# Optimization experiments

Measured on AMD Instinct MI355X. Metric: run time of the kernel, lower is better.

## Reference

```python
import jax, jax.numpy as jnp
import numpy as np

N_NODES = 50000


def _sage_max(x, src, dst, W_l, b_l, W_r):
    # gather neighbor (source) features, scatter-max to destination nodes
    msgs = x[src]                                   # [E, F]
    agg = jax.ops.segment_max(msgs, dst, num_segments=N_NODES)  # [N, F], -inf for empty
    agg = jnp.where(jnp.isneginf(agg), 0.0, agg)    # PyG fills isolated nodes with 0
    return agg @ W_l + b_l + x @ W_r                # lin_l(aggr) + lin_r(x)


def setup_inputs() -> dict:
    key = jax.random.key(0)
    ks = jax.random.split(key, 9)
    F_IN, H, OUT, E, EL = 128, 256, 32, 800000, 200000
    x = jax.random.normal(ks[0], (N_NODES, F_IN), dtype=jnp.float32)
    edge_index = jax.random.randint(ks[1], (2, E), 0, N_NODES, dtype=jnp.int64)
    edge_label_index = jax.random.randint(ks[2], (2, EL), 0, N_NODES, dtype=jnp.int64)
    s1 = 1.0 / np.sqrt(F_IN)
    s2 = 1.0 / np.sqrt(H)
    W1_l = jax.random.normal(ks[3], (F_IN, H), dtype=jnp.float32) * s1
    b1 = jnp.zeros((H,), dtype=jnp.float32)
    W1_r = jax.random.normal(ks[4], (F_IN, H), dtype=jnp.float32) * s1
    W2_l = jax.random.normal(ks[5], (H, OUT), dtype=jnp.float32) * s2
    b2 = jnp.zeros((OUT,), dtype=jnp.float32)
    W2_r = jax.random.normal(ks[6], (H, OUT), dtype=jnp.float32) * s2
    return {"x": x, "edge_index": edge_index, "edge_label_index": edge_label_index,
            "W1_l": W1_l, "b1": b1, "W1_r": W1_r,
            "W2_l": W2_l, "b2": b2, "W2_r": W2_r}


def reference(x, edge_index, edge_label_index, W1_l, b1, W1_r, W2_l, b2, W2_r):
    src, dst = edge_index[0], edge_index[1]
    # encode (eval mode: dropout is identity)
    h = jax.nn.relu(_sage_max(x, src, dst, W1_l, b1, W1_r))
    z = _sage_max(h, src, dst, W2_l, b2, W2_r)       # [N, 32]
    # decode: dot product between endpoint embeddings
    s = z[edge_label_index[0]]
    d = z[edge_label_index[1]]
    return jnp.sum(s * d, axis=-1)                   # [E_label]
```

## Files before the change

kernel.cpp:

```cpp
#include <hip/hip_runtime.h>
#include <hip/hip_bf16.h>
#include <math.h>

#define N_NODES 50000
#define NBKT 196
#define BSH 8
#define TILE2 4096
#define CAP 64
#define P2CAP 5888
#define SCAN_FLAG 0x40000000

typedef __attribute__((ext_vector_type(8))) short short8;
typedef __attribute__((ext_vector_type(4))) float f32x4;

static __device__ __forceinline__ float b2f(unsigned int u16) {
    union { unsigned int i; float f; } c; c.i = u16 << 16; return c.f;
}
static __device__ __forceinline__ unsigned int fbits(float f) {
    union { float f; unsigned int i; } c; c.f = f; return c.i;
}
static __device__ __forceinline__ unsigned short f2b_rne(float f) {
    unsigned int u = fbits(f);
    u += 0x7fff + ((u >> 16) & 1);
    return (unsigned short)(u >> 16);
}

static __device__ __forceinline__ unsigned char quant8(float v) {
    int q = (int)(v * 15.9375f + 0.5f);
    return (unsigned char)min(q, 255);
}
static __device__ __forceinline__ float dequant8(int b) {
    return (float)b * 0.0627451f;
}


__global__ __launch_bounds__(256) void k_prepbin(
        const float* __restrict__ x, unsigned short* __restrict__ xb,
        const float* __restrict__ W1l, const float* __restrict__ W1r, unsigned short* __restrict__ wt1,
        const float* __restrict__ W2l, const float* __restrict__ W2r, unsigned short* __restrict__ wt2,
        const int* __restrict__ src, const int* __restrict__ dst, int E,
        uint2* __restrict__ tmp, int* __restrict__ cnts, int ntile) {
    __shared__ int cnt[256], sstart[256], lcur[256];
    __shared__ uint2 stage[TILE2];
    const int CX = (N_NODES * 128 / 4) / 256;
    const int CW = CX + 320;
    int b = blockIdx.x, t = threadIdx.x;
    if (b < CX) {
        int i = b * 256 + t;
        float4 v = *(const float4*)(x + (size_t)i * 4);
        ushort4 o;
        o.x = f2b_rne(v.x); o.y = f2b_rne(v.y); o.z = f2b_rne(v.z); o.w = f2b_rne(v.w);
        *(ushort4*)(xb + (size_t)i * 4) = o;
    } else if (b < CX + 256) {
        int i = (b - CX) * 256 + t;
        int n = i >> 8, k = i & 255;
        float v = (k < 128) ? W1l[(size_t)k * 256 + n] : W1r[(size_t)(k - 128) * 256 + n];
        wt1[(size_t)n * 256 + k] = f2b_rne(v);
    } else if (b < CW) {
        int i = (b - CX - 256) * 256 + t;
        int n = i >> 9, k = i & 511;
        float v = (k < 256) ? W2l[(size_t)k * 32 + n] : W2r[(size_t)(k - 256) * 32 + n];
        wt2[(size_t)n * 512 + k] = f2b_rne(v);
    } else {
        int tb = b - CW;
        int e0 = tb * TILE2;
        int tilecnt = min(TILE2, E - e0);
        if (tilecnt <= 0) return;
        cnt[t] = 0;
        __syncthreads();
        if (tilecnt == TILE2) {
            for (int i = 4 * t; i < TILE2; i += 1024) {
                int4 d = *(const int4*)(dst + e0 + i);
                atomicAdd(&cnt[d.x >> BSH], 1);
                atomicAdd(&cnt[d.y >> BSH], 1);
                atomicAdd(&cnt[d.z >> BSH], 1);
                atomicAdd(&cnt[d.w >> BSH], 1);
            }
        } else {
            for (int i = t; i < tilecnt; i += 256)
                atomicAdd(&cnt[dst[e0 + i] >> BSH], 1);
        }
        __syncthreads();
        int cv = cnt[t];
        sstart[t] = cv;
        __syncthreads();
        for (int off = 1; off < 256; off <<= 1) {
            int add = (t >= off) ? sstart[t - off] : 0;
            __syncthreads();
            sstart[t] += add;
            __syncthreads();
        }
        int mystart = sstart[t] - cv;
        __syncthreads();
        sstart[t] = mystart;
        lcur[t] = mystart;
        __syncthreads();
        if (tilecnt == TILE2) {
            for (int i = 4 * t; i < TILE2; i += 1024) {
                int4 d = *(const int4*)(dst + e0 + i);
                int4 s = *(const int4*)(src + e0 + i);
                int q0 = atomicAdd(&lcur[d.x >> BSH], 1); stage[q0] = (uint2){(unsigned)s.x, (unsigned)d.x};
                int q1 = atomicAdd(&lcur[d.y >> BSH], 1); stage[q1] = (uint2){(unsigned)s.y, (unsigned)d.y};
                int q2 = atomicAdd(&lcur[d.z >> BSH], 1); stage[q2] = (uint2){(unsigned)s.z, (unsigned)d.z};
                int q3 = atomicAdd(&lcur[d.w >> BSH], 1); stage[q3] = (uint2){(unsigned)s.w, (unsigned)d.w};
            }
        } else {
            for (int i = t; i < tilecnt; i += 256) {
                int d = dst[e0 + i];
                int s = src[e0 + i];
                int q = atomicAdd(&lcur[d >> BSH], 1);
                uint2 p; p.x = (unsigned)s; p.y = (unsigned)d;
                stage[q] = p;
            }
        }
        __syncthreads();
        if (t < NBKT) cnts[(size_t)t * ntile + tb] = cnt[t];
        for (int i = t; i < tilecnt; i += 256) {
            uint2 p = stage[i];
            int bk = (int)(p.y >> BSH);
            tmp[((size_t)bk * ntile + tb) * CAP + (i - sstart[bk])] = p;
        }
    }
}


__global__ __launch_bounds__(256) void k_bin2(const uint2* __restrict__ tmp,
        const int* __restrict__ cnts, int* __restrict__ pub,
        int* __restrict__ rowptr, int* __restrict__ esrc, int N, int E, int ntile) {
    __shared__ int sc[256], toff[260], nodecnt[256], lcur[256];
    __shared__ int stage[P2CAP];
    __shared__ int shsum[4];
    int k = blockIdx.x, t = threadIdx.x;

    int c = (t < ntile) ? cnts[(size_t)k * ntile + t] : 0;
    sc[t] = c;
    __syncthreads();
    for (int off = 1; off < 256; off <<= 1) {
        int add = (t >= off) ? sc[t - off] : 0;
        __syncthreads();
        sc[t] += add;
        __syncthreads();
    }
    if (t < ntile) toff[t] = sc[t] - c;
    if (t == 255) toff[ntile] = sc[255];
    __syncthreads();
    int total = toff[ntile];

    if (t == 255) atomicExch(&pub[k], SCAN_FLAG | total);
    int v = 0;
    if (t < k) {
        int val;
        do { val = atomicOr(&pub[t], 0); } while (!(val & SCAN_FLAG) || (val & 0x80000000));
        v = val & (SCAN_FLAG - 1);
    }
#pragma unroll
    for (int off = 32; off >= 1; off >>= 1) v += __shfl_xor(v, off);
    if ((t & 63) == 0) shsum[t >> 6] = v;
    nodecnt[t] = 0;
    __syncthreads();
    int base = shsum[0] + shsum[1] + shsum[2] + shsum[3];

    for (int i = t; i < total; i += 256) {
        int lo = 0, hi = ntile;
        while (hi - lo > 1) { int mid = (lo + hi) >> 1; if (toff[mid] <= i) lo = mid; else hi = mid; }
        uint2 p = tmp[((size_t)k * ntile + lo) * CAP + (i - toff[lo])];
        atomicAdd(&nodecnt[(int)p.y & 255], 1);
    }
    __syncthreads();

    int nc = nodecnt[t];
    sc[t] = nc;
    __syncthreads();
    for (int off = 1; off < 256; off <<= 1) {
        int add = (t >= off) ? sc[t - off] : 0;
        __syncthreads();
        sc[t] += add;
        __syncthreads();
    }
    int ex = sc[t] - nc;
    int node = (k << BSH) + t;
    if (node < N) rowptr[node] = base + ex;
    if (node == N) rowptr[N] = E;
    lcur[t] = ex;
    __syncthreads();

    if (total <= P2CAP) {
        for (int i = t; i < total; i += 256) {
            int lo = 0, hi = ntile;
            while (hi - lo > 1) { int mid = (lo + hi) >> 1; if (toff[mid] <= i) lo = mid; else hi = mid; }
            uint2 p = tmp[((size_t)k * ntile + lo) * CAP + (i - toff[lo])];
            int q = atomicAdd(&lcur[(int)p.y & 255], 1);
            stage[q] = (int)p.x;
        }
        __syncthreads();
        for (int i = t; i < total; i += 256)
            esrc[base + i] = stage[i];
    } else {
        for (int i = t; i < total; i += 256) {
            int lo = 0, hi = ntile;
            while (hi - lo > 1) { int mid = (lo + hi) >> 1; if (toff[mid] <= i) lo = mid; else hi = mid; }
            uint2 p = tmp[((size_t)k * ntile + lo) * CAP + (i - toff[lo])];
            int q = atomicAdd(&lcur[(int)p.y & 255], 1);
            esrc[base + q] = (int)p.x;
        }
    }
}


__global__ __launch_bounds__(256) void k_seg_max1(const unsigned short* __restrict__ feat,
        const int* __restrict__ rowptr, const int* __restrict__ esrc,
        unsigned short* __restrict__ out) {
    int w = threadIdx.x >> 6, t = threadIdx.x & 63;
    int n = blockIdx.x * 4 + w;
    int lane16 = t & 15, sub = t >> 4;
    int beg = rowptr[n], end = rowptr[n + 1];
    float m[8];
#pragma unroll
    for (int k = 0; k < 8; ++k) m[k] = -INFINITY;
    for (int base = beg; base < end; base += 64) {
        int cnt = min(64, end - base);
        int vidx = (base + t < end) ? __builtin_nontemporal_load(&esrc[base + t]) : 0;
        for (int j = 0; j < cnt; j += 16) {
            uint4 v[4];
#pragma unroll
            for (int u = 0; u < 4; ++u) {
                int e = min(j + 4 * u + sub, cnt - 1);
                int s = __shfl(vidx, e);
                v[u] = *(const uint4*)(feat + (size_t)s * 128 + lane16 * 8);
            }
#pragma unroll
            for (int u = 0; u < 4; ++u) {
                m[0] = fmaxf(m[0], b2f(v[u].x & 0xffff));
                m[1] = fmaxf(m[1], b2f(v[u].x >> 16));
                m[2] = fmaxf(m[2], b2f(v[u].y & 0xffff));
                m[3] = fmaxf(m[3], b2f(v[u].y >> 16));
                m[4] = fmaxf(m[4], b2f(v[u].z & 0xffff));
                m[5] = fmaxf(m[5], b2f(v[u].z >> 16));
                m[6] = fmaxf(m[6], b2f(v[u].w & 0xffff));
                m[7] = fmaxf(m[7], b2f(v[u].w >> 16));
            }
        }
    }
#pragma unroll
    for (int k = 0; k < 8; ++k) {
        m[k] = fmaxf(m[k], __shfl_xor(m[k], 16));
        m[k] = fmaxf(m[k], __shfl_xor(m[k], 32));
        if (beg == end) m[k] = 0.f;
    }
    if (sub == 0) {
        uint4 p;
        p.x = (fbits(m[0]) >> 16) | (fbits(m[1]) & 0xffff0000u);
        p.y = (fbits(m[2]) >> 16) | (fbits(m[3]) & 0xffff0000u);
        p.z = (fbits(m[4]) >> 16) | (fbits(m[5]) & 0xffff0000u);
        p.w = (fbits(m[6]) >> 16) | (fbits(m[7]) & 0xffff0000u);
        *(uint4*)(out + (size_t)n * 128 + lane16 * 8) = p;
    }
}


__global__ __launch_bounds__(256) void k_seg_max2(const unsigned char* __restrict__ feat8,
        const int* __restrict__ rowptr, const int* __restrict__ esrc,
        unsigned short* __restrict__ out) {
    int w = threadIdx.x >> 6, t = threadIdx.x & 63;
    int n = blockIdx.x * 4 + w;
    int lane16 = t & 15, sub = t >> 4;
    int beg = rowptr[n], end = rowptr[n + 1];
    int m[16];
#pragma unroll
    for (int k = 0; k < 16; ++k) m[k] = 0;
    for (int base = beg; base < end; base += 64) {
        int cnt = min(64, end - base);
        int vidx = (base + t < end) ? __builtin_nontemporal_load(&esrc[base + t]) : 0;
        for (int j = 0; j < cnt; j += 32) {
            uint4 v[8];
#pragma unroll
            for (int u = 0; u < 8; ++u) {
                int e = min(j + 4 * u + sub, cnt - 1);
                int s = __shfl(vidx, e);
                v[u] = *(const uint4*)(feat8 + (size_t)s * 256 + lane16 * 16);
            }
#pragma unroll
            for (int u = 0; u < 8; ++u) {
                m[0]  = max(m[0],  (int)(v[u].x & 0xFF));
                m[1]  = max(m[1],  (int)((v[u].x >> 8) & 0xFF));
                m[2]  = max(m[2],  (int)((v[u].x >> 16) & 0xFF));
                m[3]  = max(m[3],  (int)(v[u].x >> 24));
                m[4]  = max(m[4],  (int)(v[u].y & 0xFF));
                m[5]  = max(m[5],  (int)((v[u].y >> 8) & 0xFF));
                m[6]  = max(m[6],  (int)((v[u].y >> 16) & 0xFF));
                m[7]  = max(m[7],  (int)(v[u].y >> 24));
                m[8]  = max(m[8],  (int)(v[u].z & 0xFF));
                m[9]  = max(m[9],  (int)((v[u].z >> 8) & 0xFF));
                m[10] = max(m[10], (int)((v[u].z >> 16) & 0xFF));
                m[11] = max(m[11], (int)(v[u].z >> 24));
                m[12] = max(m[12], (int)(v[u].w & 0xFF));
                m[13] = max(m[13], (int)((v[u].w >> 8) & 0xFF));
                m[14] = max(m[14], (int)((v[u].w >> 16) & 0xFF));
                m[15] = max(m[15], (int)(v[u].w >> 24));
            }
        }
    }
#pragma unroll
    for (int k = 0; k < 16; ++k) {
        m[k] = max(m[k], __shfl_xor(m[k], 16));
        m[k] = max(m[k], __shfl_xor(m[k], 32));
    }
    if (sub == 0) {
        unsigned int pk[8];
#pragma unroll
        for (int k = 0; k < 8; ++k) {
            float f0 = dequant8(m[2 * k]);
            float f1 = dequant8(m[2 * k + 1]);
            pk[k] = (fbits(f0) >> 16) | (fbits(f1) & 0xffff0000u);
        }
        uint4 a, b;
        a.x = pk[0]; a.y = pk[1]; a.z = pk[2]; a.w = pk[3];
        b.x = pk[4]; b.y = pk[5]; b.z = pk[6]; b.w = pk[7];
        *(uint4*)(out + (size_t)n * 256 + lane16 * 16) = a;
        *(uint4*)(out + (size_t)n * 256 + lane16 * 16 + 8) = b;
    }
}


__global__ __launch_bounds__(256) void k_lin1_mfma(
        const unsigned short* __restrict__ A0, const unsigned short* __restrict__ A1,
        const unsigned short* __restrict__ WT, const float* __restrict__ bias,
        unsigned short* __restrict__ H, unsigned char* __restrict__ H8, int M) {
    __shared__ short As[128 * 40];
    __shared__ short Bs[128 * 40];

    int tid = threadIdx.x;
    int m0 = blockIdx.y * 128, n0 = blockIdx.x * 128;
    int L = tid & 63, wv = tid >> 6;
    int wr = wv >> 1, wc = wv & 1;
    int lane16 = L & 15, q = L >> 4;

    f32x4 acc[4][4];
#pragma unroll
    for (int i = 0; i < 4; ++i)
#pragma unroll
        for (int j = 0; j < 4; ++j) acc[i][j] = (f32x4){0.f, 0.f, 0.f, 0.f};

    for (int k0 = 0; k0 < 256; k0 += 32) {
        const unsigned short* Abase = (k0 < 128) ? A0 : A1;
        int kc = k0 & 127;
#pragma unroll
        for (int s = tid; s < 512; s += 256) {
            int m = s >> 2, sg = s & 3;
            int row = m0 + m;
            float4 v = {0.f, 0.f, 0.f, 0.f};
            if (row < M) v = *(const float4*)(Abase + (size_t)row * 128 + kc + sg * 8);
            *(float4*)&As[m * 40 + sg * 8] = v;
        }
#pragma unroll
        for (int s = tid; s < 512; s += 256) {
            int n = s >> 2, sg = s & 3;
            *(float4*)&Bs[n * 40 + sg * 8] =
                *(const float4*)(WT + (size_t)(n0 + n) * 256 + k0 + sg * 8);
        }
        __syncthreads();

        short8 a[4], b[4];
#pragma unroll
        for (int i = 0; i < 4; ++i)
            a[i] = *(const short8*)&As[(wr * 64 + i * 16 + lane16) * 40 + q * 8];
#pragma unroll
        for (int j = 0; j < 4; ++j)
            b[j] = *(const short8*)&Bs[(wc * 64 + j * 16 + lane16) * 40 + q * 8];
#pragma unroll
        for (int i = 0; i < 4; ++i)
#pragma unroll
            for (int j = 0; j < 4; ++j)
                acc[i][j] = __builtin_amdgcn_mfma_f32_16x16x32_bf16(a[i], b[j], acc[i][j], 0, 0, 0);
        __syncthreads();
    }

#pragma unroll
    for (int i = 0; i < 4; ++i) {
#pragma unroll
        for (int r = 0; r < 4; ++r) {
            int row = m0 + wr * 64 + i * 16 + q * 4 + r;
            if (row >= M) continue;
#pragma unroll
            for (int j = 0; j < 4; ++j) {
                int col = n0 + wc * 64 + j * 16 + lane16;
                float v = fmaxf(acc[i][j][r] + bias[col], 0.f);
                H[(size_t)row * 256 + col] = f2b_rne(v);
                H8[(size_t)row * 256 + col] = quant8(v);
            }
        }
    }
}


__global__ __launch_bounds__(256) void k_lin2_mfma(
        const unsigned short* __restrict__ A0, const unsigned short* __restrict__ A1,
        const unsigned short* __restrict__ WT, const float* __restrict__ bias,
        float* __restrict__ Z, int M) {
    __shared__ short As[128 * 40];
    __shared__ short Bs[32 * 40];

    int tid = threadIdx.x;
    int m0 = blockIdx.x * 128;
    int L = tid & 63, wv = tid >> 6;
    int lane16 = L & 15, q = L >> 4;

    f32x4 acc[2][2];
#pragma unroll
    for (int i = 0; i < 2; ++i)
#pragma unroll
        for (int j = 0; j < 2; ++j) acc[i][j] = (f32x4){0.f, 0.f, 0.f, 0.f};

    for (int k0 = 0; k0 < 512; k0 += 32) {
        const unsigned short* Abase = (k0 < 256) ? A0 : A1;
        int kc = k0 & 255;
#pragma unroll
        for (int s = tid; s < 512; s += 256) {
            int m = s >> 2, sg = s & 3;
            int row = m0 + m;
            float4 v = {0.f, 0.f, 0.f, 0.f};
            if (row < M) v = *(const float4*)(Abase + (size_t)row * 256 + kc + sg * 8);
            *(float4*)&As[m * 40 + sg * 8] = v;
        }
        if (tid < 128) {
            int n = tid >> 2, sg = tid & 3;
            *(float4*)&Bs[n * 40 + sg * 8] =
                *(const float4*)(WT + (size_t)n * 512 + k0 + sg * 8);
        }
        __syncthreads();

        short8 a[2], b[2];
#pragma unroll
        for (int i = 0; i < 2; ++i)
            a[i] = *(const short8*)&As[(wv * 32 + i * 16 + lane16) * 40 + q * 8];
#pragma unroll
        for (int j = 0; j < 2; ++j)
            b[j] = *(const short8*)&Bs[(j * 16 + lane16) * 40 + q * 8];
#pragma unroll
        for (int i = 0; i < 2; ++i)
#pragma unroll
            for (int j = 0; j < 2; ++j)
                acc[i][j] = __builtin_amdgcn_mfma_f32_16x16x32_bf16(a[i], b[j], acc[i][j], 0, 0, 0);
        __syncthreads();
    }

#pragma unroll
    for (int i = 0; i < 2; ++i) {
#pragma unroll
        for (int r = 0; r < 4; ++r) {
            int row = m0 + wv * 32 + i * 16 + q * 4 + r;
            if (row >= M) continue;
#pragma unroll
            for (int j = 0; j < 2; ++j) {
                int col = j * 16 + lane16;
                Z[(size_t)row * 32 + col] = acc[i][j][r] + bias[col];
            }
        }
    }
}


__global__ void k_decode(const float* __restrict__ z, const int* __restrict__ eli,
                         int EL, float* __restrict__ out) {
    int tid = blockIdx.x * blockDim.x + threadIdx.x;
    int e = tid >> 3, lane = tid & 7;
    if (e >= EL) return;
    int s = eli[e], d = eli[EL + e];
    float4 a = *((const float4*)(z + (size_t)s * 32) + lane);
    float4 b = *((const float4*)(z + (size_t)d * 32) + lane);
    float dot = a.x * b.x + a.y * b.y + a.z * b.z + a.w * b.w;
    dot += __shfl_xor(dot, 1);
    dot += __shfl_xor(dot, 2);
    dot += __shfl_xor(dot, 4);
    if (lane == 0) out[e] = dot;
}


extern "C" void kernel_launch(void* const* d_in, const int* in_sizes, int n_in,
                              void* d_out, int out_size, void* d_ws, size_t ws_size,
                              hipStream_t stream) {
    const float* x   = (const float*)d_in[0];
    const int*   ei  = (const int*)d_in[1];
    const int*   eli = (const int*)d_in[2];
    const float* W1l = (const float*)d_in[3];
    const float* b1  = (const float*)d_in[4];
    const float* W1r = (const float*)d_in[5];
    const float* W2l = (const float*)d_in[6];
    const float* b2  = (const float*)d_in[7];
    const float* W2r = (const float*)d_in[8];
    float* out = (float*)d_out;

    int N  = N_NODES;
    int E  = in_sizes[1] / 2;
    int EL = in_sizes[2] / 2;
    const int* src = ei;
    const int* dst = ei + E;

    char* ws = (char*)d_ws;
    size_t off = 0;
    auto alloc = [&](size_t bytes) -> void* {
        void* p = ws + off;
        off += (bytes + 255) & ~(size_t)255;
        return p;
    };
    unsigned short* xb   = (unsigned short*)alloc((size_t)N * 128 * 2);
    unsigned short* aggb = (unsigned short*)alloc((size_t)N * 256 * 2);
    unsigned short* hb   = (unsigned short*)alloc((size_t)N * 256 * 2);
    unsigned char*  h8   = (unsigned char*)alloc((size_t)N * 256);
    float* zbuf          = (float*)alloc((size_t)N * 32 * 4);
    unsigned short* wt1  = (unsigned short*)alloc(256 * 256 * 2);
    unsigned short* wt2  = (unsigned short*)alloc(32 * 512 * 2);
    int* rowptr   = (int*)alloc((size_t)(N + 1) * 4);
    int ntile     = (E + TILE2 - 1) / TILE2;
    int* cnts     = (int*)alloc((size_t)NBKT * ntile * 4);
    int* pub      = (int*)alloc(256 * 4);
    int* esrc     = (int*)alloc((size_t)E * 4);
    uint2* tmpp   = (uint2*)aggb;

    const int tb = 256;
    const int CW = 6250 + 320;

    k_prepbin<<<CW + ntile, tb, 0, stream>>>(x, xb, W1l, W1r, wt1, W2l, W2r, wt2,
                                             src, dst, E, tmpp, cnts, ntile);
    k_bin2<<<NBKT, tb, 0, stream>>>(tmpp, cnts, pub, rowptr, esrc, N, E, ntile);

    k_seg_max1<<<(N + 3) / 4, tb, 0, stream>>>(xb, rowptr, esrc, aggb);
    dim3 g1(2, (N + 127) / 128);
    k_lin1_mfma<<<g1, tb, 0, stream>>>(aggb, xb, wt1, b1, hb, h8, N);

    k_seg_max2<<<(N + 3) / 4, tb, 0, stream>>>(h8, rowptr, esrc, aggb);
    k_lin2_mfma<<<(N + 127) / 128, tb, 0, stream>>>(aggb, hb, wt2, b2, zbuf, N);

    k_decode<<<(EL * 8 + 255) / 256, tb, 0, stream>>>(zbuf, eli, EL, out);
}
```

Measured before the change: 255.3 us.

## Fuse h@W2_r into layer-1 GEMM epilogue and keep layer-2 aggregate in uint8

The layer-1 GEMM epilogue now keeps the relu'd bf16 tile in shared memory and immediately multiplies it by the matching slice of W2_r, atomically accumulating partial z into a zero-initialised buffer. This removes the bf16 H write and its later re-read by the layer-2 GEMM, which now only handles the aggregated half (K=256). The layer-2 segment max writes packed uint8 instead of dequantised bf16, and the layer-2 GEMM dequantises on load. Costs added are float atomics on z, a zeroing pass folded into the prep kernel, and extra shared memory in the layer-1 GEMM, which may reduce occupancy.

```diff
diff --git a/kernel.cpp b/kernel.cpp
--- a/kernel.cpp
+++ b/kernel.cpp
@@ -38,12 +38,14 @@
         const float* __restrict__ x, unsigned short* __restrict__ xb,
         const float* __restrict__ W1l, const float* __restrict__ W1r, unsigned short* __restrict__ wt1,
         const float* __restrict__ W2l, const float* __restrict__ W2r, unsigned short* __restrict__ wt2,
+        float* __restrict__ zb,
         const int* __restrict__ src, const int* __restrict__ dst, int E,
         uint2* __restrict__ tmp, int* __restrict__ cnts, int ntile) {
     __shared__ int cnt[256], sstart[256], lcur[256];
     __shared__ uint2 stage[TILE2];
     const int CX = (N_NODES * 128 / 4) / 256;
     const int CW = CX + 320;
+    const int CZ = CW + 1563;
     int b = blockIdx.x, t = threadIdx.x;
     if (b < CX) {
         int i = b * 256 + t;
@@ -61,8 +63,11 @@
         int n = i >> 9, k = i & 511;
         float v = (k < 256) ? W2l[(size_t)k * 32 + n] : W2r[(size_t)(k - 256) * 32 + n];
         wt2[(size_t)n * 512 + k] = f2b_rne(v);
+    } else if (b < CZ) {
+        int i = (b - CW) * 256 + t;
+        if (i < 400000) ((float4*)zb)[i] = (float4){0.f, 0.f, 0.f, 0.f};
     } else {
-        int tb = b - CW;
+        int tb = b - CZ;
         int e0 = tb * TILE2;
         int tilecnt = min(TILE2, E - e0);
         if (tilecnt <= 0) return;
@@ -260,7 +265,7 @@
 
 __global__ __launch_bounds__(256) void k_seg_max2(const unsigned char* __restrict__ feat8,
         const int* __restrict__ rowptr, const int* __restrict__ esrc,
-        unsigned short* __restrict__ out) {
+        unsigned char* __restrict__ out8) {
     int w = threadIdx.x >> 6, t = threadIdx.x & 63;
     int n = blockIdx.x * 4 + w;
     int lane16 = t & 15, sub = t >> 4;
@@ -306,18 +311,12 @@
         m[k] = max(m[k], __shfl_xor(m[k], 32));
     }
     if (sub == 0) {
-        unsigned int pk[8];
-#pragma unroll
-        for (int k = 0; k < 8; ++k) {
-            float f0 = dequant8(m[2 * k]);
-            float f1 = dequant8(m[2 * k + 1]);
-            pk[k] = (fbits(f0) >> 16) | (fbits(f1) & 0xffff0000u);
-        }
-        uint4 a, b;
-        a.x = pk[0]; a.y = pk[1]; a.z = pk[2]; a.w = pk[3];
-        b.x = pk[4]; b.y = pk[5]; b.z = pk[6]; b.w = pk[7];
-        *(uint4*)(out + (size_t)n * 256 + lane16 * 16) = a;
-        *(uint4*)(out + (size_t)n * 256 + lane16 * 16 + 8) = b;
+        uint4 p;
+        p.x = m[0]  | (m[1]  << 8) | (m[2]  << 16) | (m[3]  << 24);
+        p.y = m[4]  | (m[5]  << 8) | (m[6]  << 16) | (m[7]  << 24);
+        p.z = m[8]  | (m[9]  << 8) | (m[10] << 16) | (m[11] << 24);
+        p.w = m[12] | (m[13] << 8) | (m[14] << 16) | (m[15] << 24);
+        *(uint4*)(out8 + (size_t)n * 256 + lane16 * 16) = p;
     }
 }
 
@@ -325,15 +324,27 @@
 __global__ __launch_bounds__(256) void k_lin1_mfma(
         const unsigned short* __restrict__ A0, const unsigned short* __restrict__ A1,
         const unsigned short* __restrict__ WT, const float* __restrict__ bias,
-        unsigned short* __restrict__ H, unsigned char* __restrict__ H8, int M) {
-    __shared__ short As[128 * 40];
-    __shared__ short Bs[128 * 40];
+        const unsigned short* __restrict__ WT2, float* __restrict__ zpart,
+        unsigned char* __restrict__ H8, int M) {
+    __shared__ short sh[16640];
+    __shared__ short Bs2[32 * 136];
+    short* As = sh;
+    short* Bs = sh + 5120;
+    short* Hs = sh;
 
     int tid = threadIdx.x;
     int m0 = blockIdx.y * 128, n0 = blockIdx.x * 128;
     int L = tid & 63, wv = tid >> 6;
     int wr = wv >> 1, wc = wv & 1;
     int lane16 = L & 15, q = L >> 4;
+
+    {
+        int n = tid >> 3, kc = (tid & 7) * 16;
+        *(float4*)&Bs2[n * 136 + kc] =
+            *(const float4*)(WT2 + (size_t)n * 512 + 256 + n0 + kc);
+        *(float4*)&Bs2[n * 136 + kc + 8] =
+            *(const float4*)(WT2 + (size_t)n * 512 + 256 + n0 + kc + 8);
+    }
 
     f32x4 acc[4][4];
 #pragma unroll
@@ -379,14 +390,51 @@
     for (int i = 0; i < 4; ++i) {
 #pragma unroll
         for (int r = 0; r < 4; ++r) {
-            int row = m0 + wr * 64 + i * 16 + q * 4 + r;
+            int lrow = wr * 64 + i * 16 + q * 4 + r;
+            int row = m0 + lrow;
+#pragma unroll
+            for (int j = 0; j < 4; ++j) {
+                int lcol = wc * 64 + j * 16 + lane16;
+                int col = n0 + lcol;
+                float v = fmaxf(acc[i][j][r] + bias[col], 0.f);
+                unsigned short hb16 = f2b_rne(v);
+                Hs[lrow * 130 + lcol] = (short)hb16;
+                if (row < M) H8[(size_t)row * 256 + col] = quant8(v);
+            }
+        }
+    }
+    __syncthreads();
+
+    f32x4 acc2[2][2];
+#pragma unroll
+    for (int i = 0; i < 2; ++i)
+#pragma unroll
+        for (int j = 0; j < 2; ++j) acc2[i][j] = (f32x4){0.f, 0.f, 0.f, 0.f};
+#pragma unroll
+    for (int kk = 0; kk < 4; ++kk) {
+        short8 a2[2], b2[2];
+#pragma unroll
+        for (int i = 0; i < 2; ++i)
+            a2[i] = *(const short8*)&Hs[(wv * 32 + i * 16 + lane16) * 130 + kk * 32 + q * 8];
+#pragma unroll
+        for (int j = 0; j < 2; ++j)
+            b2[j] = *(const short8*)&Bs2[(j * 16 + lane16) * 136 + kk * 32 + q * 8];
+#pragma unroll
+        for (int i = 0; i < 2; ++i)
+#pragma unroll
+            for (int j = 0; j < 2; ++j)
+                acc2[i][j] = __builtin_amdgcn_mfma_f32_16x16x32_bf16(a2[i], b2[j], acc2[i][j], 0, 0, 0);
+    }
+#pragma unroll
+    for (int i = 0; i < 2; ++i) {
+#pragma unroll
+        for (int r = 0; r < 4; ++r) {
+            int row = m0 + wv * 32 + i * 16 + q * 4 + r;
             if (row >= M) continue;
 #pragma unroll
-            for (int j = 0; j < 4; ++j) {
-                int col = n0 + wc * 64 + j * 16 + lane16;
-                float v = fmaxf(acc[i][j][r] + bias[col], 0.f);
-                H[(size_t)row * 256 + col] = f2b_rne(v);
-                H8[(size_t)row * 256 + col] = quant8(v);
+            for (int j = 0; j < 2; ++j) {
+                int col = j * 16 + lane16;
+                atomicAdd(&zpart[(size_t)row * 32 + col], acc2[i][j][r]);
             }
         }
     }
@@ -394,7 +442,7 @@
 
 
 __global__ __launch_bounds__(256) void k_lin2_mfma(
-        const unsigned short* __restrict__ A0, const unsigned short* __restrict__ A1,
+        const unsigned char* __restrict__ A8,
         const unsigned short* __restrict__ WT, const float* __restrict__ bias,
         float* __restrict__ Z, int M) {
     __shared__ short As[128 * 40];
@@ -411,16 +459,26 @@
 #pragma unroll
         for (int j = 0; j < 2; ++j) acc[i][j] = (f32x4){0.f, 0.f, 0.f, 0.f};
 
-    for (int k0 = 0; k0 < 512; k0 += 32) {
-        const unsigned short* Abase = (k0 < 256) ? A0 : A1;
-        int kc = k0 & 255;
+    for (int k0 = 0; k0 < 256; k0 += 32) {
 #pragma unroll
         for (int s = tid; s < 512; s += 256) {
             int m = s >> 2, sg = s & 3;
             int row = m0 + m;
-            float4 v = {0.f, 0.f, 0.f, 0.f};
-            if (row < M) v = *(const float4*)(Abase + (size_t)row * 256 + kc + sg * 8);
-            *(float4*)&As[m * 40 + sg * 8] = v;
+            uint2 v8 = {0u, 0u};
+            if (row < M) v8 = *(const uint2*)(A8 + (size_t)row * 256 + k0 + sg * 8);
+            unsigned short e[8];
+#pragma unroll
+            for (int bi = 0; bi < 4; ++bi)
+                e[bi] = f2b_rne((float)((v8.x >> (8 * bi)) & 255u) * 0.0627451f);
+#pragma unroll
+            for (int bi = 0; bi < 4; ++bi)
+                e[4 + bi] = f2b_rne((float)((v8.y >> (8 * bi)) & 255u) * 0.0627451f);
+            uint4 p;
+            p.x = e[0] | ((unsigned)e[1] << 16);
+            p.y = e[2] | ((unsigned)e[3] << 16);
+            p.z = e[4] | ((unsigned)e[5] << 16);
+            p.w = e[6] | ((unsigned)e[7] << 16);
+            *(uint4*)&As[m * 40 + sg * 8] = p;
         }
         if (tid < 128) {
             int n = tid >> 2, sg = tid & 3;
@@ -453,7 +511,8 @@
 #pragma unroll
             for (int j = 0; j < 2; ++j) {
                 int col = j * 16 + lane16;
-                Z[(size_t)row * 32 + col] = acc[i][j][r] + bias[col];
+                float zp = Z[(size_t)row * 32 + col];
+                Z[(size_t)row * 32 + col] = acc[i][j][r] + bias[col] + zp;
             }
         }
     }
@@ -505,7 +564,6 @@
     };
     unsigned short* xb   = (unsigned short*)alloc((size_t)N * 128 * 2);
     unsigned short* aggb = (unsigned short*)alloc((size_t)N * 256 * 2);
-    unsigned short* hb   = (unsigned short*)alloc((size_t)N * 256 * 2);
     unsigned char*  h8   = (unsigned char*)alloc((size_t)N * 256);
     float* zbuf          = (float*)alloc((size_t)N * 32 * 4);
     unsigned short* wt1  = (unsigned short*)alloc(256 * 256 * 2);
@@ -516,20 +574,21 @@
     int* pub      = (int*)alloc(256 * 4);
     int* esrc     = (int*)alloc((size_t)E * 4);
     uint2* tmpp   = (uint2*)aggb;
+    unsigned char* agg8 = (unsigned char*)aggb;
 
     const int tb = 256;
-    const int CW = 6250 + 320;
-
-    k_prepbin<<<CW + ntile, tb, 0, stream>>>(x, xb, W1l, W1r, wt1, W2l, W2r, wt2,
+    const int CZ = 6250 + 320 + 1563;
+
+    k_prepbin<<<CZ + ntile, tb, 0, stream>>>(x, xb, W1l, W1r, wt1, W2l, W2r, wt2, zbuf,
                                              src, dst, E, tmpp, cnts, ntile);
     k_bin2<<<NBKT, tb, 0, stream>>>(tmpp, cnts, pub, rowptr, esrc, N, E, ntile);
 
     k_seg_max1<<<(N + 3) / 4, tb, 0, stream>>>(xb, rowptr, esrc, aggb);
     dim3 g1(2, (N + 127) / 128);
-    k_lin1_mfma<<<g1, tb, 0, stream>>>(aggb, xb, wt1, b1, hb, h8, N);
-
-    k_seg_max2<<<(N + 3) / 4, tb, 0, stream>>>(h8, rowptr, esrc, aggb);
-    k_lin2_mfma<<<(N + 127) / 128, tb, 0, stream>>>(aggb, hb, wt2, b2, zbuf, N);
+    k_lin1_mfma<<<g1, tb, 0, stream>>>(aggb, xb, wt1, b1, wt2, zbuf, h8, N);
+
+    k_seg_max2<<<(N + 3) / 4, tb, 0, stream>>>(h8, rowptr, esrc, agg8);
+    k_lin2_mfma<<<(N + 127) / 128, tb, 0, stream>>>(agg8, wt2, b2, zbuf, N);
 
     k_decode<<<(EL * 8 + 255) / 256, tb, 0, stream>>>(zbuf, eli, EL, out);
 }
```

Measured after the change: 253.0 us. No clear change (-0.9%).
